# Kernel tuning notes

Measured on AMD Instinct MI355X. Metric: run time of the kernel, lower is better.

The kernel has to match this reference:

```python
import jax, jax.numpy as jnp
import numpy as np

N_QUBITS = 4
DIM = 2 ** N_QUBITS
N_LAYERS = 5

# PennyLane default.qubit: wire 0 is the most significant bit of the state index.
_bits = ((np.arange(DIM)[None, :] >> (N_QUBITS - 1 - np.arange(N_QUBITS)[:, None])) & 1)  # [4,16]
Z_SIGNS = jnp.asarray(1.0 - 2.0 * _bits, dtype=jnp.float32)                                # [4,16] +1/-1

def _cz_sign(a, b):
    s = np.where((_bits[a] == 1) & (_bits[b] == 1), -1.0, 1.0)
    return jnp.asarray(s, dtype=jnp.complex64)  # [16]

CZ_SIGNS = [_cz_sign(i, i + 1) for i in range(N_QUBITS - 1)] + [_cz_sign(N_QUBITS - 1, 0)]

def apply_1q(psi, U, w):
    # psi: [B,16] complex; U: [2,2] or [B,2,2]; wire w (0 = MSB)
    L, R = 2 ** w, 2 ** (N_QUBITS - 1 - w)
    psi = psi.reshape(-1, L, 2, R)
    if U.ndim == 2:
        out = jnp.einsum('ij,bljr->blir', U, psi)
    else:
        out = jnp.einsum('bij,bljr->blir', U, psi)
    return out.reshape(-1, DIM)

def _mat(a, b, c, d):
    return jnp.stack([jnp.stack([a, b], -1), jnp.stack([c, d], -1)], -2)  # [B,2,2]

def ry_gate(t):
    c, s = jnp.cos(t / 2).astype(jnp.complex64), jnp.sin(t / 2).astype(jnp.complex64)
    return _mat(c, -s, s, c)

def rz_gate(t):
    e = jnp.exp(-0.5j * t.astype(jnp.complex64))
    z = jnp.zeros_like(e)
    return _mat(e, z, z, jnp.conj(e))

def rx_gate(t):
    c = jnp.cos(t / 2).astype(jnp.complex64)
    s = (-1j) * jnp.sin(t / 2).astype(jnp.complex64)
    return _mat(c, s, s, c)

H_GATE = jnp.asarray(np.array([[1, 1], [1, -1]]) / np.sqrt(2.0), dtype=jnp.complex64)

def quantum_batch(params, xy):
    # params: [B, n_layers, 2*n_qubits]; xy: [B,2] -> expvals [B,4]
    B = xy.shape[0]
    psi = jnp.zeros((B, DIM), jnp.complex64).at[:, 0].set(1.0)
    pi = jnp.float32(np.pi)
    for i in range(N_QUBITS):
        psi = apply_1q(psi, H_GATE, i)
        psi = apply_1q(psi, ry_gate(xy[:, 0] * pi), i)
        psi = apply_1q(psi, rz_gate(xy[:, 1] * pi), i)
    for l in range(N_LAYERS):
        ang = params[:, l, :]  # [B,8]
        for i in range(N_QUBITS):
            psi = apply_1q(psi, rx_gate(ang[:, i]), i)
            psi = apply_1q(psi, ry_gate(ang[:, i + N_QUBITS]), i)
        for s in CZ_SIGNS:
            psi = psi * s[None, :]
    probs = jnp.abs(psi) ** 2  # [B,16]
    return probs @ Z_SIGNS.T   # [B,4]

def setup_inputs() -> dict:
    key = jax.random.key(0)
    ks = jax.random.split(key, 9)
    B = 131072
    def lin(k, fin, fout):
        bound = 1.0 / np.sqrt(fin)
        k1, k2 = jax.random.split(k)
        W = jax.random.uniform(k1, (fin, fout), jnp.float32, -bound, bound)
        b = jax.random.uniform(k2, (fout,), jnp.float32, -bound, bound)
        return W, b
    W1, b1 = lin(ks[0], 2, 16)
    W2, b2 = lin(ks[1], 16, 2 * N_QUBITS * N_LAYERS)
    W3, b3 = lin(ks[2], N_QUBITS, 8)
    W4, b4 = lin(ks[3], 8, 1)
    xy = jax.random.uniform(ks[4], (B, 2), jnp.float32)
    return {"xy": xy, "W1": W1, "b1": b1, "W2": W2, "b2": b2,
            "W3": W3, "b3": b3, "W4": W4, "b4": b4}

def reference(xy, W1, b1, W2, b2, W3, b3, W4, b4):
    h = jnp.tanh(xy @ W1 + b1)
    params = jnp.tanh(h @ W2 + b2).reshape(-1, N_LAYERS, 2 * N_QUBITS)
    q = quantum_batch(params, xy)            # [B,4]
    out = jnp.tanh(q @ W3 + b3) @ W4 + b4    # [B,1]
    return out
```

## Files before the change

kernel.cpp:

```cpp
#include <hip/hip_runtime.h>

#ifndef M_PI
#define M_PI 3.14159265358979323846
#endif

typedef float v2f __attribute__((ext_vector_type(2)));

__device__ __forceinline__ v2f vfma(v2f a, v2f b, v2f c) {
    return __builtin_elementwise_fma(a, b, c);
}
__device__ __forceinline__ v2f splat(float x) { v2f r; r.x = x; r.y = x; return r; }

__device__ __forceinline__ float rcp_fast(float x) { return __builtin_amdgcn_rcpf(x); }

__device__ __forceinline__ float tanh_fast(float x) {
    float e = __expf(-2.0f * x);
    return (1.0f - e) * rcp_fast(1.0f + e);
}

__device__ __forceinline__ void cmul(float ar, float ai, float br, float bi,
                                     float& cr, float& ci) {
    cr = ar * br - ai * bi;
    ci = ar * bi + ai * br;
}

template<int K>
__device__ __forceinline__ void rx_gate_p(v2f (&sr)[8], v2f (&si)[8], float s, float c) {
    v2f cs = splat(c), ss = splat(s);
    #pragma unroll
    for (int k = 0; k < 8; ++k) {
        if ((k & K) == 0) {
            const int e = k + K;
            v2f ar = sr[k], ai = si[k], br = sr[e], bi = si[e];
            sr[k] = vfma(cs, ar,  ss * bi);
            si[k] = vfma(cs, ai, -(ss * br));
            sr[e] = vfma(cs, br,  ss * ai);
            si[e] = vfma(cs, bi, -(ss * ar));
        }
    }
}
template<int K>
__device__ __forceinline__ void ry_gate_p(v2f (&sr)[8], v2f (&si)[8], float s, float c) {
    v2f cs = splat(c), ss = splat(s);
    #pragma unroll
    for (int k = 0; k < 8; ++k) {
        if ((k & K) == 0) {
            const int e = k + K;
            v2f ar = sr[k], ai = si[k], br = sr[e], bi = si[e];
            sr[k] = vfma(cs, ar, -(ss * br));
            si[k] = vfma(cs, ai, -(ss * bi));
            sr[e] = vfma(ss, ar,  cs * br);
            si[e] = vfma(ss, ai,  cs * bi);
        }
    }
}
__device__ __forceinline__ void rx_gate_1(v2f (&sr)[8], v2f (&si)[8], float s, float c) {
    v2f cs = splat(c), ss = splat(s);
    #pragma unroll
    for (int k = 0; k < 8; ++k) {
        v2f r = sr[k], i = si[k];
        sr[k] = vfma(cs, r,  ss * i.yx);
        si[k] = vfma(cs, i, -(ss * r.yx));
    }
}
__device__ __forceinline__ void ry_gate_1(v2f (&sr)[8], v2f (&si)[8], float s, float c) {
    v2f cs = splat(c);
    v2f sn; sn.x = -s; sn.y = s;
    #pragma unroll
    for (int k = 0; k < 8; ++k) {
        v2f r = sr[k], i = si[k];
        sr[k] = vfma(cs, r, sn * r.yx);
        si[k] = vfma(cs, i, sn * i.yx);
    }
}

__global__ void __launch_bounds__(256)
qpinn_kernel(const float* __restrict__ xy,
             const float* __restrict__ W1, const float* __restrict__ b1,
             const float* __restrict__ W2, const float* __restrict__ b2,
             const float* __restrict__ W3, const float* __restrict__ b3,
             const float* __restrict__ W4, const float* __restrict__ b4,
             float* __restrict__ out, int B)
{
    int t = blockIdx.x * blockDim.x + threadIdx.x;
    if (t >= B) return;

    float2 P = reinterpret_cast<const float2*>(xy)[t];
    float x = P.x, y = P.y;

    float h[16];
    #pragma unroll
    for (int j = 0; j < 16; ++j)
        h[j] = tanh_fast(fmaf(x, W1[j], fmaf(y, W1[16 + j], b1[j])));

    float sa = __builtin_amdgcn_sinf(0.25f * x), ca = __builtin_amdgcn_cosf(0.25f * x);
    float sb = __builtin_amdgcn_sinf(0.25f * y), cb = __builtin_amdgcn_cosf(0.25f * y);
    const float is2 = 0.70710678118654752f;
    float m0 = is2 * (ca - sa), m1 = is2 * (ca + sa);
    float u0r = m0 * cb, u0i = -m0 * sb;
    float u1r = m1 * cb, u1i =  m1 * sb;

    float p2r, p2i, p3r, p3i, p4r, p4i;
    float q2r, q2i, q3r, q3i, q4r, q4i;
    cmul(u0r, u0i, u0r, u0i, p2r, p2i);
    cmul(p2r, p2i, u0r, u0i, p3r, p3i);
    cmul(p3r, p3i, u0r, u0i, p4r, p4i);
    cmul(u1r, u1i, u1r, u1i, q2r, q2i);
    cmul(q2r, q2i, u1r, u1i, q3r, q3i);
    cmul(q3r, q3i, u1r, u1i, q4r, q4i);

    float trr[5], tii[5];
    trr[0] = p4r; tii[0] = p4i;
    cmul(p3r, p3i, u1r, u1i, trr[1], tii[1]);
    cmul(p2r, p2i, q2r, q2i, trr[2], tii[2]);
    cmul(u0r, u0i, q3r, q3i, trr[3], tii[3]);
    trr[4] = q4r; tii[4] = q4i;

    constexpr int pc[16] = {0,1,1,2, 1,2,2,3, 1,2,2,3, 2,3,3,4};
    v2f sr[8], si[8];
    #pragma unroll
    for (int k = 0; k < 8; ++k) {
        sr[k].x = trr[pc[2*k]];   sr[k].y = trr[pc[2*k+1]];
        si[k].x = tii[pc[2*k]];   si[k].y = tii[pc[2*k+1]];
    }

    const float REV = 0.5f * 0.15915494309189535f;

    #pragma unroll
    for (int l = 0; l < 5; ++l) {
        float a8[8];
        #pragma unroll
        for (int m2 = 0; m2 < 4; ++m2) {
            const int j = l * 8 + 2 * m2;
            v2f acc; acc.x = b2[j]; acc.y = b2[j + 1];
            #pragma unroll
            for (int k = 0; k < 16; ++k) {
                v2f w; w.x = W2[k * 40 + j]; w.y = W2[k * 40 + j + 1];
                acc = vfma(splat(h[k]), w, acc);
            }
            a8[2*m2]     = tanh_fast(acc.x);
            a8[2*m2 + 1] = tanh_fast(acc.y);
        }

        float s, c, rev;
        rev = a8[0] * REV; s = __builtin_amdgcn_sinf(rev); c = __builtin_amdgcn_cosf(rev);
        rx_gate_p<4>(sr, si, s, c);
        rev = a8[4] * REV; s = __builtin_amdgcn_sinf(rev); c = __builtin_amdgcn_cosf(rev);
        ry_gate_p<4>(sr, si, s, c);
        rev = a8[1] * REV; s = __builtin_amdgcn_sinf(rev); c = __builtin_amdgcn_cosf(rev);
        rx_gate_p<2>(sr, si, s, c);
        rev = a8[5] * REV; s = __builtin_amdgcn_sinf(rev); c = __builtin_amdgcn_cosf(rev);
        ry_gate_p<2>(sr, si, s, c);
        rev = a8[2] * REV; s = __builtin_amdgcn_sinf(rev); c = __builtin_amdgcn_cosf(rev);
        rx_gate_p<1>(sr, si, s, c);
        rev = a8[6] * REV; s = __builtin_amdgcn_sinf(rev); c = __builtin_amdgcn_cosf(rev);
        ry_gate_p<1>(sr, si, s, c);
        rev = a8[3] * REV; s = __builtin_amdgcn_sinf(rev); c = __builtin_amdgcn_cosf(rev);
        rx_gate_1(sr, si, s, c);
        rev = a8[7] * REV; s = __builtin_amdgcn_sinf(rev); c = __builtin_amdgcn_cosf(rev);
        ry_gate_1(sr, si, s, c);

        sr[1].y = -sr[1].y;  si[1].y = -si[1].y;
        sr[3].x = -sr[3].x;  si[3].x = -si[3].x;
        sr[4].y = -sr[4].y;  si[4].y = -si[4].y;
        sr[6].x = -sr[6].x;  si[6].x = -si[6].x;
    }

    float ev[8], ov[8];
    #pragma unroll
    for (int k = 0; k < 8; ++k) {
        v2f pz = vfma(sr[k], sr[k], si[k] * si[k]);
        ev[k] = pz.x + pz.y;
        ov[k] = pz.x - pz.y;
    }
    float q0 = 0.f, q1 = 0.f, q2 = 0.f, q3 = 0.f;
    #pragma unroll
    for (int k = 0; k < 8; ++k) {
        q0 += (k & 4) ? -ev[k] : ev[k];
        q1 += (k & 2) ? -ev[k] : ev[k];
        q2 += (k & 1) ? -ev[k] : ev[k];
        q3 += ov[k];
    }

    float oacc = b4[0];
    #pragma unroll
    for (int j2 = 0; j2 < 4; ++j2) {
        const int j = 2 * j2;
        v2f g;  g.x = b3[j];  g.y = b3[j + 1];
        v2f w;
        w.x = W3[j];      w.y = W3[j + 1];       g = vfma(splat(q0), w, g);
        w.x = W3[8 + j];  w.y = W3[8 + j + 1];   g = vfma(splat(q1), w, g);
        w.x = W3[16 + j]; w.y = W3[16 + j + 1];  g = vfma(splat(q2), w, g);
        w.x = W3[24 + j]; w.y = W3[24 + j + 1];  g = vfma(splat(q3), w, g);
        oacc = fmaf(tanh_fast(g.x), W4[j],     oacc);
        oacc = fmaf(tanh_fast(g.y), W4[j + 1], oacc);
    }
    out[t] = oacc;
}

extern "C" void kernel_launch(void* const* d_in, const int* in_sizes, int n_in,
                              void* d_out, int out_size, void* d_ws, size_t ws_size,
                              hipStream_t stream) {
    const float* xy = (const float*)d_in[0];
    const float* W1 = (const float*)d_in[1];
    const float* b1 = (const float*)d_in[2];
    const float* W2 = (const float*)d_in[3];
    const float* b2 = (const float*)d_in[4];
    const float* W3 = (const float*)d_in[5];
    const float* b3 = (const float*)d_in[6];
    const float* W4 = (const float*)d_in[7];
    const float* b4 = (const float*)d_in[8];
    float* out = (float*)d_out;

    const int B = in_sizes[0] / 2;
    const int block = 256;
    const int grid = (B + block - 1) / block;
    qpinn_kernel<<<grid, block, 0, stream>>>(xy, W1, b1, W2, b2, W3, b3, W4, b4, out, B);
}
```

Baseline: 17.01 us.

## Split each sample's statevector across two lanes with DPP exchanges

Each batch sample now runs on a pair of threads. Each thread holds half of the 16-amplitude state, the wire-0 gate is done through DPP quad-permute swaps, and the W2 matvec, the sin/cos work and the final reduction are split across the pair with partial results exchanged. W2 is staged in shared memory in a reordered layout so it can be read with float4 loads, and launch bounds request more occupancy. This cuts per-thread register pressure and serial ALU work in exchange for twice as many threads, cross-lane shuffles, a shared-memory staging step and a barrier per block. It also relies on the `if (t >= B) return` early exit happening after `__syncthreads`, which holds here.

```diff
diff --git a/kernel.cpp b/kernel.cpp
--- a/kernel.cpp
+++ b/kernel.cpp
@@ -1,8 +1,4 @@
 #include <hip/hip_runtime.h>
-
-#ifndef M_PI
-#define M_PI 3.14159265358979323846
-#endif
 
 typedef float v2f __attribute__((ext_vector_type(2)));
 
@@ -24,11 +20,20 @@
     ci = ar * bi + ai * br;
 }
 
+__device__ __forceinline__ float pswap(float v) {
+    int i = __builtin_bit_cast(int, v);
+    i = __builtin_amdgcn_mov_dpp(i, 0xB1, 0xF, 0xF, true);
+    return __builtin_bit_cast(float, i);
+}
+__device__ __forceinline__ v2f pswap2(v2f v) {
+    v2f r; r.x = pswap(v.x); r.y = pswap(v.y); return r;
+}
+
 template<int K>
-__device__ __forceinline__ void rx_gate_p(v2f (&sr)[8], v2f (&si)[8], float s, float c) {
+__device__ __forceinline__ void rx_local(v2f (&sr)[4], v2f (&si)[4], float s, float c) {
     v2f cs = splat(c), ss = splat(s);
     #pragma unroll
-    for (int k = 0; k < 8; ++k) {
+    for (int k = 0; k < 4; ++k) {
         if ((k & K) == 0) {
             const int e = k + K;
             v2f ar = sr[k], ai = si[k], br = sr[e], bi = si[e];
@@ -40,10 +45,10 @@
     }
 }
 template<int K>
-__device__ __forceinline__ void ry_gate_p(v2f (&sr)[8], v2f (&si)[8], float s, float c) {
+__device__ __forceinline__ void ry_local(v2f (&sr)[4], v2f (&si)[4], float s, float c) {
     v2f cs = splat(c), ss = splat(s);
     #pragma unroll
-    for (int k = 0; k < 8; ++k) {
+    for (int k = 0; k < 4; ++k) {
         if ((k & K) == 0) {
             const int e = k + K;
             v2f ar = sr[k], ai = si[k], br = sr[e], bi = si[e];
@@ -54,27 +59,27 @@
         }
     }
 }
-__device__ __forceinline__ void rx_gate_1(v2f (&sr)[8], v2f (&si)[8], float s, float c) {
+__device__ __forceinline__ void rx_1(v2f (&sr)[4], v2f (&si)[4], float s, float c) {
     v2f cs = splat(c), ss = splat(s);
     #pragma unroll
-    for (int k = 0; k < 8; ++k) {
+    for (int k = 0; k < 4; ++k) {
         v2f r = sr[k], i = si[k];
         sr[k] = vfma(cs, r,  ss * i.yx);
         si[k] = vfma(cs, i, -(ss * r.yx));
     }
 }
-__device__ __forceinline__ void ry_gate_1(v2f (&sr)[8], v2f (&si)[8], float s, float c) {
+__device__ __forceinline__ void ry_1(v2f (&sr)[4], v2f (&si)[4], float s, float c) {
     v2f cs = splat(c);
     v2f sn; sn.x = -s; sn.y = s;
     #pragma unroll
-    for (int k = 0; k < 8; ++k) {
+    for (int k = 0; k < 4; ++k) {
         v2f r = sr[k], i = si[k];
         sr[k] = vfma(cs, r, sn * r.yx);
         si[k] = vfma(cs, i, sn * i.yx);
     }
 }
 
-__global__ void __launch_bounds__(256)
+__global__ void __launch_bounds__(256, 4)
 qpinn_kernel(const float* __restrict__ xy,
              const float* __restrict__ W1, const float* __restrict__ b1,
              const float* __restrict__ W2, const float* __restrict__ b2,
@@ -82,16 +87,41 @@
              const float* __restrict__ W4, const float* __restrict__ b4,
              float* __restrict__ out, int B)
 {
-    int t = blockIdx.x * blockDim.x + threadIdx.x;
+    __shared__ __align__(16) float w2s[640];
+    for (int i = threadIdx.x; i < 640; i += 256) {
+        int c = i & 1, k = (i >> 1) & 15, m2 = (i >> 5) & 3, l = i >> 7;
+        w2s[i] = W2[k * 40 + l * 8 + m2 * 2 + c];
+    }
+    __syncthreads();
+
+    int tid = blockIdx.x * 256 + threadIdx.x;
+    int t = tid >> 1;
+    int p = tid & 1;
     if (t >= B) return;
+
+    const float psign = p ? 1.0f : -1.0f;
 
     float2 P = reinterpret_cast<const float2*>(xy)[t];
     float x = P.x, y = P.y;
 
-    float h[16];
-    #pragma unroll
-    for (int j = 0; j < 16; ++j)
-        h[j] = tanh_fast(fmaf(x, W1[j], fmaf(y, W1[16 + j], b1[j])));
+    const int j0 = 8 * p;
+    float4 w1xa = *(const float4*)(W1 + j0);
+    float4 w1xb = *(const float4*)(W1 + j0 + 4);
+    float4 w1ya = *(const float4*)(W1 + 16 + j0);
+    float4 w1yb = *(const float4*)(W1 + 16 + j0 + 4);
+    float4 b1a  = *(const float4*)(b1 + j0);
+    float4 b1b  = *(const float4*)(b1 + j0 + 4);
+    float hl[8], hq[8];
+    hl[0] = tanh_fast(fmaf(x, w1xa.x, fmaf(y, w1ya.x, b1a.x)));
+    hl[1] = tanh_fast(fmaf(x, w1xa.y, fmaf(y, w1ya.y, b1a.y)));
+    hl[2] = tanh_fast(fmaf(x, w1xa.z, fmaf(y, w1ya.z, b1a.z)));
+    hl[3] = tanh_fast(fmaf(x, w1xa.w, fmaf(y, w1ya.w, b1a.w)));
+    hl[4] = tanh_fast(fmaf(x, w1xb.x, fmaf(y, w1yb.x, b1b.x)));
+    hl[5] = tanh_fast(fmaf(x, w1xb.y, fmaf(y, w1yb.y, b1b.y)));
+    hl[6] = tanh_fast(fmaf(x, w1xb.z, fmaf(y, w1yb.z, b1b.z)));
+    hl[7] = tanh_fast(fmaf(x, w1xb.w, fmaf(y, w1yb.w, b1b.w)));
+    #pragma unroll
+    for (int jj = 0; jj < 8; ++jj) hq[jj] = pswap(hl[jj]);
 
     float sa = __builtin_amdgcn_sinf(0.25f * x), ca = __builtin_amdgcn_cosf(0.25f * x);
     float sb = __builtin_amdgcn_sinf(0.25f * y), cb = __builtin_amdgcn_cosf(0.25f * y);
@@ -99,103 +129,140 @@
     float m0 = is2 * (ca - sa), m1 = is2 * (ca + sa);
     float u0r = m0 * cb, u0i = -m0 * sb;
     float u1r = m1 * cb, u1i =  m1 * sb;
-
-    float p2r, p2i, p3r, p3i, p4r, p4i;
-    float q2r, q2i, q3r, q3i, q4r, q4i;
-    cmul(u0r, u0i, u0r, u0i, p2r, p2i);
-    cmul(p2r, p2i, u0r, u0i, p3r, p3i);
-    cmul(p3r, p3i, u0r, u0i, p4r, p4i);
-    cmul(u1r, u1i, u1r, u1i, q2r, q2i);
-    cmul(q2r, q2i, u1r, u1i, q3r, q3i);
-    cmul(q3r, q3i, u1r, u1i, q4r, q4i);
-
-    float trr[5], tii[5];
-    trr[0] = p4r; tii[0] = p4i;
-    cmul(p3r, p3i, u1r, u1i, trr[1], tii[1]);
-    cmul(p2r, p2i, q2r, q2i, trr[2], tii[2]);
-    cmul(u0r, u0i, q3r, q3i, trr[3], tii[3]);
-    trr[4] = q4r; tii[4] = q4i;
-
-    constexpr int pc[16] = {0,1,1,2, 1,2,2,3, 1,2,2,3, 2,3,3,4};
-    v2f sr[8], si[8];
-    #pragma unroll
-    for (int k = 0; k < 8; ++k) {
-        sr[k].x = trr[pc[2*k]];   sr[k].y = trr[pc[2*k+1]];
-        si[k].x = tii[pc[2*k]];   si[k].y = tii[pc[2*k+1]];
-    }
+    float a2r, a2i, bb2r, bb2i;
+    cmul(u0r, u0i, u0r, u0i, a2r, a2i);
+    cmul(u1r, u1i, u1r, u1i, bb2r, bb2i);
+    float t0r, t0i, t1r, t1i, t2r, t2i, t3r, t3i;
+    cmul(a2r, a2i, u0r, u0i, t0r, t0i);
+    cmul(a2r, a2i, u1r, u1i, t1r, t1i);
+    cmul(bb2r, bb2i, u0r, u0i, t2r, t2i);
+    cmul(bb2r, bb2i, u1r, u1i, t3r, t3i);
+    float wr = p ? u1r : u0r, wi = p ? u1i : u0i;
+    v2f sr[4], si[4];
+    {
+        v2f pr[4] = {{t0r, t1r}, {t1r, t2r}, {t1r, t2r}, {t2r, t3r}};
+        v2f pi[4] = {{t0i, t1i}, {t1i, t2i}, {t1i, t2i}, {t2i, t3i}};
+        v2f wrv = splat(wr), wiv = splat(wi);
+        #pragma unroll
+        for (int k = 0; k < 4; ++k) {
+            sr[k] = vfma(wrv, pr[k], -(wiv * pi[k]));
+            si[k] = vfma(wrv, pi[k],  wiv * pr[k]);
+        }
+    }
+
+    v2f czA; czA.x = 1.0f; czA.y = -psign;
+    v2f czB; czB.x = 1.0f; czB.y =  psign;
+    v2f czC; czC.x = -psign; czC.y = 1.0f;
+    v2f czD; czD.x =  psign; czD.y = 1.0f;
 
     const float REV = 0.5f * 0.15915494309189535f;
 
     #pragma unroll
     for (int l = 0; l < 5; ++l) {
-        float a8[8];
-        #pragma unroll
-        for (int m2 = 0; m2 < 4; ++m2) {
-            const int j = l * 8 + 2 * m2;
-            v2f acc; acc.x = b2[j]; acc.y = b2[j + 1];
+        float4 b2v = *(const float4*)(b2 + l * 8 + 4 * p);
+        v2f acc0; acc0.x = b2v.x; acc0.y = b2v.y;
+        v2f acc1; acc1.x = b2v.z; acc1.y = b2v.w;
+        const float* blk0 = w2s + (l * 4 + 2 * p) * 32;
+        const float* blk1 = blk0 + 32;
+        const int own = 16 * p, par = 16 - 16 * p;
+        #pragma unroll
+        for (int kk = 0; kk < 8; kk += 2) {
+            float4 wA = *(const float4*)(blk0 + own + 2 * kk);
+            float4 wB = *(const float4*)(blk1 + own + 2 * kk);
+            v2f wAlo; wAlo.x = wA.x; wAlo.y = wA.y;
+            v2f wAhi; wAhi.x = wA.z; wAhi.y = wA.w;
+            v2f wBlo; wBlo.x = wB.x; wBlo.y = wB.y;
+            v2f wBhi; wBhi.x = wB.z; wBhi.y = wB.w;
+            acc0 = vfma(splat(hl[kk]),     wAlo, acc0);
+            acc0 = vfma(splat(hl[kk + 1]), wAhi, acc0);
+            acc1 = vfma(splat(hl[kk]),     wBlo, acc1);
+            acc1 = vfma(splat(hl[kk + 1]), wBhi, acc1);
+        }
+        #pragma unroll
+        for (int kk = 0; kk < 8; kk += 2) {
+            float4 wA = *(const float4*)(blk0 + par + 2 * kk);
+            float4 wB = *(const float4*)(blk1 + par + 2 * kk);
+            v2f wAlo; wAlo.x = wA.x; wAlo.y = wA.y;
+            v2f wAhi; wAhi.x = wA.z; wAhi.y = wA.w;
+            v2f wBlo; wBlo.x = wB.x; wBlo.y = wB.y;
+            v2f wBhi; wBhi.x = wB.z; wBhi.y = wB.w;
+            acc0 = vfma(splat(hq[kk]),     wAlo, acc0);
+            acc0 = vfma(splat(hq[kk + 1]), wAhi, acc0);
+            acc1 = vfma(splat(hq[kk]),     wBlo, acc1);
+            acc1 = vfma(splat(hq[kk + 1]), wBhi, acc1);
+        }
+        float aown[4];
+        aown[0] = tanh_fast(acc0.x);
+        aown[1] = tanh_fast(acc0.y);
+        aown[2] = tanh_fast(acc1.x);
+        aown[3] = tanh_fast(acc1.y);
+        float apar[4];
+        #pragma unroll
+        for (int w = 0; w < 4; ++w) apar[w] = pswap(aown[w]);
+        float sx[4], cx[4], sy[4], cy[4];
+        #pragma unroll
+        for (int w = 0; w < 4; ++w) {
+            float arx = p ? apar[w] : aown[w];
+            float ary = p ? aown[w] : apar[w];
+            float r1 = arx * REV, r2 = ary * REV;
+            sx[w] = __builtin_amdgcn_sinf(r1); cx[w] = __builtin_amdgcn_cosf(r1);
+            sy[w] = __builtin_amdgcn_sinf(r2); cy[w] = __builtin_amdgcn_cosf(r2);
+        }
+
+        {
+            float aR = cy[0] * cx[0], aI = sy[0] * sx[0];
+            float bR = sy[0] * cx[0], bI = -(cy[0] * sx[0]);
+            float A2 = psign * aI, B1 = psign * bR;
+            v2f aRv = splat(aR), A2v = splat(A2), B1v = splat(B1), bIv = splat(bI);
             #pragma unroll
-            for (int k = 0; k < 16; ++k) {
-                v2f w; w.x = W2[k * 40 + j]; w.y = W2[k * 40 + j + 1];
-                acc = vfma(splat(h[k]), w, acc);
+            for (int k = 0; k < 4; ++k) {
+                v2f qr = pswap2(sr[k]), qi = pswap2(si[k]);
+                v2f orr = sr[k], oii = si[k];
+                v2f nr = vfma(aRv, orr, vfma(A2v, oii, vfma(B1v, qr, -(bIv * qi))));
+                v2f ni = vfma(aRv, oii, vfma(-A2v, orr, vfma(B1v, qi, bIv * qr)));
+                sr[k] = nr; si[k] = ni;
             }
-            a8[2*m2]     = tanh_fast(acc.x);
-            a8[2*m2 + 1] = tanh_fast(acc.y);
-        }
-
-        float s, c, rev;
-        rev = a8[0] * REV; s = __builtin_amdgcn_sinf(rev); c = __builtin_amdgcn_cosf(rev);
-        rx_gate_p<4>(sr, si, s, c);
-        rev = a8[4] * REV; s = __builtin_amdgcn_sinf(rev); c = __builtin_amdgcn_cosf(rev);
-        ry_gate_p<4>(sr, si, s, c);
-        rev = a8[1] * REV; s = __builtin_amdgcn_sinf(rev); c = __builtin_amdgcn_cosf(rev);
-        rx_gate_p<2>(sr, si, s, c);
-        rev = a8[5] * REV; s = __builtin_amdgcn_sinf(rev); c = __builtin_amdgcn_cosf(rev);
-        ry_gate_p<2>(sr, si, s, c);
-        rev = a8[2] * REV; s = __builtin_amdgcn_sinf(rev); c = __builtin_amdgcn_cosf(rev);
-        rx_gate_p<1>(sr, si, s, c);
-        rev = a8[6] * REV; s = __builtin_amdgcn_sinf(rev); c = __builtin_amdgcn_cosf(rev);
-        ry_gate_p<1>(sr, si, s, c);
-        rev = a8[3] * REV; s = __builtin_amdgcn_sinf(rev); c = __builtin_amdgcn_cosf(rev);
-        rx_gate_1(sr, si, s, c);
-        rev = a8[7] * REV; s = __builtin_amdgcn_sinf(rev); c = __builtin_amdgcn_cosf(rev);
-        ry_gate_1(sr, si, s, c);
-
-        sr[1].y = -sr[1].y;  si[1].y = -si[1].y;
-        sr[3].x = -sr[3].x;  si[3].x = -si[3].x;
-        sr[4].y = -sr[4].y;  si[4].y = -si[4].y;
-        sr[6].x = -sr[6].x;  si[6].x = -si[6].x;
-    }
-
-    float ev[8], ov[8];
-    #pragma unroll
-    for (int k = 0; k < 8; ++k) {
-        v2f pz = vfma(sr[k], sr[k], si[k] * si[k]);
-        ev[k] = pz.x + pz.y;
-        ov[k] = pz.x - pz.y;
-    }
-    float q0 = 0.f, q1 = 0.f, q2 = 0.f, q3 = 0.f;
-    #pragma unroll
-    for (int k = 0; k < 8; ++k) {
-        q0 += (k & 4) ? -ev[k] : ev[k];
-        q1 += (k & 2) ? -ev[k] : ev[k];
-        q2 += (k & 1) ? -ev[k] : ev[k];
-        q3 += ov[k];
-    }
+        }
+        rx_local<2>(sr, si, sx[1], cx[1]);
+        ry_local<2>(sr, si, sy[1], cy[1]);
+        rx_local<1>(sr, si, sx[2], cx[2]);
+        ry_local<1>(sr, si, sy[2], cy[2]);
+        rx_1(sr, si, sx[3], cx[3]);
+        ry_1(sr, si, sy[3], cy[3]);
+
+        sr[0] = sr[0] * czA; si[0] = si[0] * czA;
+        sr[1] = sr[1] * czB; si[1] = si[1] * czB;
+        sr[2] = sr[2] * czC; si[2] = si[2] * czC;
+        sr[3] = sr[3] * czD; si[3] = si[3] * czD;
+    }
+
+    v2f pz[4];
+    #pragma unroll
+    for (int k = 0; k < 4; ++k) pz[k] = vfma(sr[k], sr[k], si[k] * si[k]);
+    float e0 = pz[0].x + pz[0].y, e1 = pz[1].x + pz[1].y;
+    float e2 = pz[2].x + pz[2].y, e3 = pz[3].x + pz[3].y;
+    float o0 = pz[0].x - pz[0].y, o1 = pz[1].x - pz[1].y;
+    float o2 = pz[2].x - pz[2].y, o3 = pz[3].x - pz[3].y;
+    float q0l = -psign * (e0 + e1 + e2 + e3);
+    float q1l = (e0 + e1) - (e2 + e3);
+    float q2l = (e0 - e1) + (e2 - e3);
+    float q3l = (o0 + o1) + (o2 + o3);
+    float q0f = q0l + pswap(q0l);
+    float q1f = q1l + pswap(q1l);
+    float q2f = q2l + pswap(q2l);
+    float q3f = q3l + pswap(q3l);
 
     float oacc = b4[0];
     #pragma unroll
-    for (int j2 = 0; j2 < 4; ++j2) {
-        const int j = 2 * j2;
-        v2f g;  g.x = b3[j];  g.y = b3[j + 1];
-        v2f w;
-        w.x = W3[j];      w.y = W3[j + 1];       g = vfma(splat(q0), w, g);
-        w.x = W3[8 + j];  w.y = W3[8 + j + 1];   g = vfma(splat(q1), w, g);
-        w.x = W3[16 + j]; w.y = W3[16 + j + 1];  g = vfma(splat(q2), w, g);
-        w.x = W3[24 + j]; w.y = W3[24 + j + 1];  g = vfma(splat(q3), w, g);
-        oacc = fmaf(tanh_fast(g.x), W4[j],     oacc);
-        oacc = fmaf(tanh_fast(g.y), W4[j + 1], oacc);
-    }
-    out[t] = oacc;
+    for (int j = 0; j < 8; ++j) {
+        float g = b3[j];
+        g = fmaf(q0f, W3[j],      g);
+        g = fmaf(q1f, W3[8 + j],  g);
+        g = fmaf(q2f, W3[16 + j], g);
+        g = fmaf(q3f, W3[24 + j], g);
+        oacc = fmaf(tanh_fast(g), W4[j], oacc);
+    }
+    if (p == 0) out[t] = oacc;
 }
 
 extern "C" void kernel_launch(void* const* d_in, const int* in_sizes, int n_in,
@@ -213,7 +280,8 @@
     float* out = (float*)d_out;
 
     const int B = in_sizes[0] / 2;
+    const int threads = 2 * B;
     const int block = 256;
-    const int grid = (B + block - 1) / block;
+    const int grid = (threads + block - 1) / block;
     qpinn_kernel<<<grid, block, 0, stream>>>(xy, W1, b1, W2, b2, W3, b3, W4, b4, out, B);
 }
```

New measurement: 19.79 us. 1.16x slower.
